# Kernel optimization log

Measured on AMD Instinct MI355X. Metric: run time of the kernel, lower is better.

The kernel has to match this reference:

```python
import jax, jax.numpy as jnp
import numpy as np

EPS = 1e-5

def conv2d(x, w, stride=1, padding=0, bias=None):
    out = jax.lax.conv_general_dilated(
        x, w, (stride, stride), [(padding, padding), (padding, padding)],
        dimension_numbers=('NCHW', 'OIHW', 'NCHW'))
    if bias is not None:
        out = out + bias[None, :, None, None]
    return out

def bn_relu(x, gamma, beta, mean, var):
    scale = gamma / jnp.sqrt(var + EPS)
    return jax.nn.relu(x * scale[None, :, None, None]
                       + (beta - mean * scale)[None, :, None, None])

def deform_conv(x, wp, bp, wc, ks, pad, stride):
    # Canonical DeformConv2d (v1, modulation=False) from pytorch-deform-conv-v2.
    b, c, H, W = x.shape
    N = ks * ks
    offset = conv2d(x, wp, stride=stride, padding=1, bias=bp)        # (b,2N,h,w)
    h, w = offset.shape[2], offset.shape[3]
    xp = jnp.pad(x, ((0, 0), (0, 0), (pad, pad), (pad, pad)))        # zero_padding
    Hp, Wp = H + 2 * pad, W + 2 * pad
    off = offset.transpose(0, 2, 3, 1)                               # (b,h,w,2N)
    rng = jnp.arange(-(ks - 1) // 2, (ks - 1) // 2 + 1, dtype=x.dtype)
    pnx, pny = jnp.meshgrid(rng, rng, indexing='ij')
    pnx, pny = pnx.reshape(-1), pny.reshape(-1)                      # (N,)
    p0x = jnp.arange(1, h * stride + 1, stride, dtype=x.dtype)       # torch starts at 1
    p0y = jnp.arange(1, w * stride + 1, stride, dtype=x.dtype)
    px = p0x[None, :, None, None] + pnx[None, None, None, :] + off[..., :N]  # (b,h,w,N)
    py = p0y[None, None, :, None] + pny[None, None, None, :] + off[..., N:]
    qx0 = jnp.floor(jax.lax.stop_gradient(px))
    qy0 = jnp.floor(jax.lax.stop_gradient(py))
    qx0c = jnp.clip(qx0, 0, Hp - 1).astype(jnp.int32)
    qx1c = jnp.clip(qx0 + 1, 0, Hp - 1).astype(jnp.int32)
    qy0c = jnp.clip(qy0, 0, Wp - 1).astype(jnp.int32)
    qy1c = jnp.clip(qy0 + 1, 0, Wp - 1).astype(jnp.int32)
    pxc = jnp.clip(px, 0, Hp - 1)
    pyc = jnp.clip(py, 0, Wp - 1)
    fx0 = qx0c.astype(x.dtype); fx1 = qx1c.astype(x.dtype)
    fy0 = qy0c.astype(x.dtype); fy1 = qy1c.astype(x.dtype)
    g_lt = (1 + (fx0 - pxc)) * (1 + (fy0 - pyc))
    g_rb = (1 - (fx1 - pxc)) * (1 - (fy1 - pyc))
    g_lb = (1 + (fx0 - pxc)) * (1 - (fy1 - pyc))
    g_rt = (1 - (fx1 - pxc)) * (1 + (fy0 - pyc))
    xf = xp.reshape(b, c, Hp * Wp)
    def gather(qx, qy):
        idx = (qx * Wp + qy).reshape(b, 1, h * w * N)
        return jnp.take_along_axis(xf, idx, axis=2).reshape(b, c, h, w, N)
    x_off = (g_lt[:, None] * gather(qx0c, qy0c)
             + g_rb[:, None] * gather(qx1c, qy1c)
             + g_lb[:, None] * gather(qx0c, qy1c)
             + g_rt[:, None] * gather(qx1c, qy0c))                   # (b,c,h,w,N)
    # stride=ks conv over the reshaped (h*ks, w*ks) map == einsum over sample slot n
    return jnp.einsum('bchwn,ocn->bohw', x_off, wc.reshape(wc.shape[0], c, N))

def setup_inputs() -> dict:
    key = jax.random.key(0)
    ks = iter(jax.random.split(key, 40))
    def nrm(shape, scale):
        return jax.random.normal(next(ks), shape, dtype=jnp.float32) * scale
    def he(shape):  # fan_in = prod of all but first dim
        return nrm(shape, float(np.sqrt(2.0 / np.prod(shape[1:]))))
    def bn(c):
        return (jnp.ones((c,), jnp.float32) + nrm((c,), 0.05),  # gamma
                nrm((c,), 0.05),                                 # beta
                nrm((c,), 0.1),                                  # running mean
                jax.random.uniform(next(ks), (c,), jnp.float32, 0.5, 1.5))  # var
    inp = {'x': jax.random.normal(next(ks), (256, 3, 32, 32), dtype=jnp.float32)}
    inp['w1'] = he((32, 3, 3, 3)); inp['b1'] = nrm((32,), 0.01)
    inp['g1'], inp['be1'], inp['m1'], inp['v1'] = bn(32)
    inp['wp2'] = nrm((18, 32, 3, 3), 0.01); inp['bp2'] = nrm((18,), 0.001)
    inp['wc2'] = he((64, 32, 3, 3))
    inp['g2'], inp['be2'], inp['m2'], inp['v2'] = bn(64)
    inp['wp3'] = nrm((18, 64, 3, 3), 0.01); inp['bp3'] = nrm((18,), 0.001)
    inp['wc3'] = he((128, 64, 3, 3))
    inp['g3'], inp['be3'], inp['m3'], inp['v3'] = bn(128)
    inp['wp4'] = nrm((18, 128, 3, 3), 0.01); inp['bp4'] = nrm((18,), 0.001)
    inp['wc4'] = he((128, 128, 3, 3))
    inp['g4'], inp['be4'], inp['m4'], inp['v4'] = bn(128)
    inp['wcls'] = nrm((100, 128), float(1.0 / np.sqrt(128)))
    inp['bcls'] = nrm((100,), 0.01)
    return inp

def reference(x, w1, b1, g1, be1, m1, v1,
              wp2, bp2, wc2, g2, be2, m2, v2,
              wp3, bp3, wc3, g3, be3, m3, v3,
              wp4, bp4, wc4, g4, be4, m4, v4,
              wcls, bcls):
    h = bn_relu(conv2d(x, w1, stride=1, padding=1, bias=b1), g1, be1, m1, v1)   # (b,32,32,32)
    h = bn_relu(deform_conv(h, wp2, bp2, wc2, 3, 1, 2), g2, be2, m2, v2)        # (b,64,16,16)
    h = bn_relu(deform_conv(h, wp3, bp3, wc3, 3, 1, 1), g3, be3, m3, v3)        # (b,128,16,16)
    h = bn_relu(deform_conv(h, wp4, bp4, wc4, 3, 1, 2), g4, be4, m4, v4)        # (b,128,8,8)
    h = jnp.mean(h, axis=(2, 3))                                                # avg_pool2d(8) -> (b,128)
    return h @ wcls.T + bcls[None, :]
```

## Files before the change

kernel.cpp:

```cpp
#include <hip/hip_runtime.h>
#include <math.h>

#define BN_EPS 1e-5f

typedef __attribute__((ext_vector_type(4))) float f4;
typedef __attribute__((ext_vector_type(4))) int i4v;
typedef __attribute__((ext_vector_type(8))) short short8;
typedef __attribute__((ext_vector_type(4))) float f32x4;

__device__ inline unsigned short f2bf(float f) {
    unsigned int u = __builtin_bit_cast(unsigned int, f);
    return (unsigned short)((u + 0x7FFFu + ((u >> 16) & 1u)) >> 16);
}
__device__ inline float blo(int u) { return __builtin_bit_cast(float, (int)(u << 16)); }
__device__ inline float bhi(int u) { return __builtin_bit_cast(float, (int)(u & 0xffff0000)); }
__device__ inline int pkbf_fast(float hi, float lo) {
    unsigned uh = __builtin_bit_cast(unsigned, hi) + 0x8000u;
    unsigned ul = __builtin_bit_cast(unsigned, lo) + 0x8000u;
    return (int)__builtin_amdgcn_perm(uh, ul, 0x07060302u);
}

struct CvtSeg { const float* src; unsigned short* dst; int oreal, c, kpad, end; };
struct CvtArgs { CvtSeg s[7]; };

__global__ __launch_bounds__(256)
void cvt_all(CvtArgs a)
{
    int idx = blockIdx.x * 256 + threadIdx.x;
    int base = 0;
    #pragma unroll
    for (int i = 0; i < 7; ++i) {
        if (idx < a.s[i].end) {
            int local = idx - base;
            int kpad = a.s[i].kpad, c = a.s[i].c;
            int o = local / kpad, k = local - o * kpad;
            unsigned short val = 0;
            if (o < a.s[i].oreal && k < 9 * c) {
                int n = k / c, cc = k - n * c;
                val = f2bf(a.s[i].src[(o * c + cc) * 9 + n]);
            }
            a.s[i].dst[local] = val;
            return;
        }
        base = a.s[i].end;
    }
}

__global__ __launch_bounds__(256)
void conv1_tile(const float* __restrict__ x, const unsigned short* __restrict__ wq,
                const float* __restrict__ bias, const float* __restrict__ g,
                const float* __restrict__ be, const float* __restrict__ m,
                const float* __restrict__ v, unsigned short* __restrict__ out)
{
    __shared__ __align__(16) float img[3072];
    __shared__ __align__(16) unsigned short wt[32 * 40];
    __shared__ float scb[32], shb[32];
    const int tid = threadIdx.x;
    const int b = blockIdx.x >> 2;
    const int qtr = blockIdx.x & 3;
    if (tid < 32) {
        float sc = g[tid] * rsqrtf(v[tid] + BN_EPS);
        scb[tid] = sc;
        shb[tid] = be[tid] - m[tid] * sc + bias[tid] * sc;
    }
    *(ushort4*)&wt[(tid >> 3) * 40 + (tid & 7) * 4] =
        *(const ushort4*)(wq + (tid >> 3) * 32 + (tid & 7) * 4);
    const float* xb = x + (size_t)b * 3072;
    #pragma unroll
    for (int r = 0; r < 3; ++r) {
        int idx = r * 256 + tid;
        *(f4*)&img[idx * 4] = *(const f4*)(xb + idx * 4);
    }
    __syncthreads();
    const int wid = tid >> 6, lane = tid & 63, quad = lane >> 4, m16 = lane & 15;
    short8 af0 = *(const short8*)&wt[m16 * 40 + quad * 8];
    short8 af1 = *(const short8*)&wt[(16 + m16) * 40 + quad * 8];
    #pragma unroll
    for (int it = 0; it < 4; ++it) {
        int pix = qtr * 256 + it * 64 + wid * 16 + m16;
        int i = pix >> 5, j = pix & 31;
        short8 bfrag;
        #pragma unroll
        for (int jj = 0; jj < 8; ++jj) {
            int k = quad * 8 + jj;
            float val = 0.f;
            if (k < 27) {
                int n = k / 3, c = k - n * 3;
                int u = i - 1 + n / 3, vv = j - 1 + n % 3;
                if (u >= 0 && u < 32 && vv >= 0 && vv < 32)
                    val = img[c * 1024 + u * 32 + vv];
            }
            bfrag[jj] = (short)f2bf(val);
        }
        f32x4 a0 = {0.f,0.f,0.f,0.f}, a1 = {0.f,0.f,0.f,0.f};
        a0 = __builtin_amdgcn_mfma_f32_16x16x32_bf16(af0, bfrag, a0, 0, 0, 0);
        a1 = __builtin_amdgcn_mfma_f32_16x16x32_bf16(af1, bfrag, a1, 0, 0, 0);
        unsigned short* op = out + ((size_t)b * 1024 + pix) * 32;
        ushort4 s0, s1;
        #pragma unroll
        for (int rr = 0; rr < 4; ++rr) {
            int o0 = quad * 4 + rr, o1 = 16 + quad * 4 + rr;
            ((unsigned short*)&s0)[rr] = f2bf(fmaxf(fmaf(a0[rr], scb[o0], shb[o0]), 0.f));
            ((unsigned short*)&s1)[rr] = f2bf(fmaxf(fmaf(a1[rr], scb[o1], shb[o1]), 0.f));
        }
        *(ushort4*)(op + quad * 4) = s0;
        *(ushort4*)(op + 16 + quad * 4) = s1;
    }
}

template<int C, int OREAL, int OPAD, int H, int W, int OH, int OW, int S,
         int MTILE, bool DEF, bool BN>
__global__ __launch_bounds__(256, 4)
void dconv(const unsigned short* __restrict__ xact, const float* __restrict__ offp,
           const unsigned short* __restrict__ wq,
           const float* __restrict__ q0, const float* __restrict__ q1,
           const float* __restrict__ q2, const float* __restrict__ q3,
           void* __restrict__ outv)
{
    constexpr int K = C * 9;
    constexpr int KCH = C / 32;
    constexpr int OSPLIT = (OPAD >= 64) ? 4 : 2;
    constexpr int G = 4 / OSPLIT;
    constexpr int OT = OPAD / (16 * OSPLIT);
    constexpr int PW = MTILE / G;
    constexpr int ST = PW / 16;
    constexpr int CP = C + 8;
    constexpr int GL = C / 8;
    constexpr int NGRP = 256 / GL;
    constexpr int NT_ITER = (MTILE + NGRP - 1) / NGRP;
    constexpr int OHW = OH * OW;
    constexpr int HWC = H * W * C;
    constexpr int Hp = H + 2, Wp = W + 2;
    static_assert(PW % 16 == 0 && OT >= 1 && MTILE % NGRP == 0, "tiling");

    __shared__ __align__(16) unsigned short xo[2][MTILE * CP];
    __shared__ __align__(16) i4v tab_i[DEF ? MTILE : 1][9];
    __shared__ __align__(16) f4  tab_w[DEF ? MTILE : 1][9];
    __shared__ int tab_o[DEF ? 1 : MTILE][9];
    __shared__ int tab_m[DEF ? 1 : MTILE][9];
    __shared__ int imgb[MTILE];
    __shared__ float scb[OPAD], shb[OPAD];

    const int tid = threadIdx.x;
    const int p0 = blockIdx.x * MTILE;

    if (tid < MTILE) imgb[tid] = ((p0 + tid) / OHW) * HWC;
    if (BN) {
        for (int o = tid; o < OREAL; o += 256) {
            float sc = q0[o] * rsqrtf(q3[o] + BN_EPS);
            scb[o] = sc;
            shb[o] = q1[o] - q2[o] * sc;
        }
    } else {
        for (int o = tid; o < OREAL; o += 256) scb[o] = q0[o];
    }

    for (int e = tid; e < MTILE * 9; e += 256) {
        int lp = e / 9, n = e % 9;
        int p = p0 + lp;
        int rem = p % OHW;
        int i = rem / OW, j = rem % OW;
        if constexpr (DEF) {
            float ox = offp[(size_t)p * 18 + n];
            float oy = offp[(size_t)p * 18 + 9 + n];
            float px = (float)(i * S + n / 3) + ox;
            float py = (float)(j * S + n % 3) + oy;
            int qx0 = (int)floorf(px), qy0 = (int)floorf(py);
            int x0 = min(max(qx0, 0), Hp - 1), x1 = min(max(qx0 + 1, 0), Hp - 1);
            int y0 = min(max(qy0, 0), Wp - 1), y1 = min(max(qy0 + 1, 0), Wp - 1);
            float pxc = fminf(fmaxf(px, 0.f), (float)(Hp - 1));
            float pyc = fminf(fmaxf(py, 0.f), (float)(Wp - 1));
            float gx0 = 1.f + ((float)x0 - pxc), gx1 = 1.f - ((float)x1 - pxc);
            float gy0 = 1.f + ((float)y0 - pyc), gy1 = 1.f - ((float)y1 - pyc);
            int u0 = x0 - 1, u1 = x1 - 1, v0 = y0 - 1, v1 = y1 - 1;
            bool k0 = (u0 >= 0 && u0 < H && v0 >= 0 && v0 < W);
            bool k1 = (u1 >= 0 && u1 < H && v1 >= 0 && v1 < W);
            bool k2 = (u0 >= 0 && u0 < H && v1 >= 0 && v1 < W);
            bool k3 = (u1 >= 0 && u1 < H && v0 >= 0 && v0 < W);
            i4v ti; f4 tw;
            ti[0] = k0 ? (u0 * W + v0) * C : 0;  tw[0] = k0 ? gx0 * gy0 : 0.f;
            ti[1] = k1 ? (u1 * W + v1) * C : 0;  tw[1] = k1 ? gx1 * gy1 : 0.f;
            ti[2] = k2 ? (u0 * W + v1) * C : 0;  tw[2] = k2 ? gx0 * gy1 : 0.f;
            ti[3] = k3 ? (u1 * W + v0) * C : 0;  tw[3] = k3 ? gx1 * gy0 : 0.f;
            tab_i[lp][n] = ti;
            tab_w[lp][n] = tw;
        } else {
            int u = i * S - 1 + n / 3, vv = j * S - 1 + n % 3;
            bool ok = (u >= 0 && u < H && vv >= 0 && vv < W);
            tab_o[lp][n] = ok ? (u * W + vv) * C : 0;
            tab_m[lp][n] = ok ? -1 : 0;
        }
    }

    const int gl = tid % GL;
    const int grp = tid / GL;
    const int wid = tid >> 6, lane = tid & 63, quad = lane >> 4, m16 = lane & 15;
    const int og = wid % OSPLIT, pg = wid / OSPLIT;
    const int obase = og * OT * 16;
    const int pixbase = pg * PW;

    auto do_gather = [&](int n, int buf) {
        #pragma unroll
        for (int it = 0; it < NT_ITER; ++it) {
            const int pix = it * NGRP + grp;
            const unsigned short* xb = xact + imgb[pix] + gl * 8;
            i4v R;
            if constexpr (DEF) {
                i4v ti = tab_i[pix][n];
                f4  tw = tab_w[pix][n];
                i4v A  = *(const i4v*)(xb + ti[0]);
                i4v Bv = *(const i4v*)(xb + ti[1]);
                i4v Cv = *(const i4v*)(xb + ti[2]);
                i4v Dv = *(const i4v*)(xb + ti[3]);
                #pragma unroll
                for (int e2 = 0; e2 < 4; ++e2) {
                    float lo = tw[0] * blo(A[e2]);
                    lo = fmaf(tw[1], blo(Bv[e2]), lo);
                    lo = fmaf(tw[2], blo(Cv[e2]), lo);
                    lo = fmaf(tw[3], blo(Dv[e2]), lo);
                    float hi = tw[0] * bhi(A[e2]);
                    hi = fmaf(tw[1], bhi(Bv[e2]), hi);
                    hi = fmaf(tw[2], bhi(Cv[e2]), hi);
                    hi = fmaf(tw[3], bhi(Dv[e2]), hi);
                    R[e2] = pkbf_fast(hi, lo);
                }
            } else {
                int mask = tab_m[pix][n];
                i4v A = *(const i4v*)(xb + tab_o[pix][n]);
                #pragma unroll
                for (int e2 = 0; e2 < 4; ++e2) R[e2] = A[e2] & mask;
            }
            *(i4v*)&xo[buf][pix * CP + gl * 8] = R;
        }
    };

    auto load_wf = [&](int n, short8 (*wf)[OT]) {
        #pragma unroll
        for (int ch = 0; ch < KCH; ++ch)
            #pragma unroll
            for (int t = 0; t < OT; ++t)
                wf[ch][t] = *(const short8*)(wq + (size_t)(obase + t * 16 + m16) * K
                                             + n * C + ch * 32 + quad * 8);
    };

    f32x4 acc[ST][OT];
    #pragma unroll
    for (int st = 0; st < ST; ++st)
        #pragma unroll
        for (int t = 0; t < OT; ++t) acc[st][t] = (f32x4){0.f, 0.f, 0.f, 0.f};

    short8 wfA[KCH][OT], wfB[KCH][OT];
    __syncthreads();
    do_gather(0, 0);
    load_wf(0, wfA);
    __syncthreads();

    for (int n = 0; n < 9; ++n) {
        const int cur = n & 1;
        if (n < 8) {
            do_gather(n + 1, cur ^ 1);
            load_wf(n + 1, wfB);
        }
        #pragma unroll
        for (int ch = 0; ch < KCH; ++ch)
            #pragma unroll
            for (int st = 0; st < ST; ++st) {
                short8 bf = *(const short8*)&xo[cur][(pixbase + st * 16 + m16) * CP
                                                    + ch * 32 + quad * 8];
                #pragma unroll
                for (int t = 0; t < OT; ++t)
                    acc[st][t] = __builtin_amdgcn_mfma_f32_16x16x32_bf16(
                        wfA[ch][t], bf, acc[st][t], 0, 0, 0);
            }
        if (n < 8) {
            #pragma unroll
            for (int ch = 0; ch < KCH; ++ch)
                #pragma unroll
                for (int t = 0; t < OT; ++t) wfA[ch][t] = wfB[ch][t];
        }
        __syncthreads();
    }

    if constexpr (BN) {
        unsigned short* outw = (unsigned short*)outv;
        #pragma unroll
        for (int st = 0; st < ST; ++st) {
            const int p = p0 + pixbase + st * 16 + m16;
            #pragma unroll
            for (int t = 0; t < OT; ++t) {
                int o = obase + t * 16 + quad * 4;
                ushort4 s;
                #pragma unroll
                for (int rr = 0; rr < 4; ++rr)
                    ((unsigned short*)&s)[rr] =
                        f2bf(fmaxf(fmaf(acc[st][t][rr], scb[o + rr], shb[o + rr]), 0.f));
                *(ushort4*)(outw + (size_t)p * OPAD + o) = s;
            }
        }
    } else {
        float* outf = (float*)outv;
        #pragma unroll
        for (int st = 0; st < ST; ++st) {
            const int p = p0 + pixbase + st * 16 + m16;
            #pragma unroll
            for (int t = 0; t < OT; ++t)
                #pragma unroll
                for (int rr = 0; rr < 4; ++rr) {
                    int o = obase + t * 16 + quad * 4 + rr;
                    if (o < OREAL)
                        outf[(size_t)p * 18 + o] = acc[st][t][rr] + scb[o];
                }
        }
    }
}

__global__ __launch_bounds__(128)
void pool_fc(const unsigned short* __restrict__ h4, const float* __restrict__ wcls,
             const float* __restrict__ bcls, float* __restrict__ out)
{
    __shared__ float pool[128];
    int b = blockIdx.x;
    int tid = threadIdx.x;
    const unsigned short* src = h4 + (size_t)b * 8192;
    float s = 0.f;
    #pragma unroll
    for (int t = 0; t < 64; ++t)
        s += __builtin_bit_cast(float, (unsigned)src[t * 128 + tid] << 16);
    pool[tid] = s * (1.f / 64.f);
    __syncthreads();
    if (tid < 100) {
        float acc = bcls[tid];
        const float* wr = wcls + tid * 128;
        #pragma unroll
        for (int c = 0; c < 128; ++c) acc = fmaf(pool[c], wr[c], acc);
        out[(size_t)b * 100 + tid] = acc;
    }
}

extern "C" void kernel_launch(void* const* d_in, const int* in_sizes, int n_in,
                              void* d_out, int out_size, void* d_ws, size_t ws_size,
                              hipStream_t stream)
{
    const float* x    = (const float*)d_in[0];
    const float* w1   = (const float*)d_in[1];
    const float* b1   = (const float*)d_in[2];
    const float* g1   = (const float*)d_in[3];
    const float* be1  = (const float*)d_in[4];
    const float* m1   = (const float*)d_in[5];
    const float* v1   = (const float*)d_in[6];
    const float* wp2  = (const float*)d_in[7];
    const float* bp2  = (const float*)d_in[8];
    const float* wc2  = (const float*)d_in[9];
    const float* g2   = (const float*)d_in[10];
    const float* be2  = (const float*)d_in[11];
    const float* m2   = (const float*)d_in[12];
    const float* v2   = (const float*)d_in[13];
    const float* wp3  = (const float*)d_in[14];
    const float* bp3  = (const float*)d_in[15];
    const float* wc3  = (const float*)d_in[16];
    const float* g3   = (const float*)d_in[17];
    const float* be3  = (const float*)d_in[18];
    const float* m3   = (const float*)d_in[19];
    const float* v3   = (const float*)d_in[20];
    const float* wp4  = (const float*)d_in[21];
    const float* bp4  = (const float*)d_in[22];
    const float* wc4  = (const float*)d_in[23];
    const float* g4   = (const float*)d_in[24];
    const float* be4  = (const float*)d_in[25];
    const float* m4   = (const float*)d_in[26];
    const float* v4   = (const float*)d_in[27];
    const float* wcls = (const float*)d_in[28];
    const float* bcls = (const float*)d_in[29];
    float* out = (float*)d_out;

    float* ws  = (float*)d_ws;
    float* off = ws;
    unsigned short* h1 = (unsigned short*)(off + 1179648);
    unsigned short* h2 = h1 + 8388608;
    unsigned short* h3 = h2 + 4194304;
    unsigned short* h4 = h3 + 8388608;
    unsigned short* wc2b = h4 + 2097152;
    unsigned short* wc3b = wc2b + 18432;
    unsigned short* wc4b = wc3b + 73728;
    unsigned short* wp2b = wc4b + 147456;
    unsigned short* wp3b = wp2b + 9216;
    unsigned short* wp4b = wp3b + 18432;
    unsigned short* wq1  = wp4b + 36864;
    (void)ws_size; (void)in_sizes; (void)n_in; (void)out_size;

    CvtArgs ca;
    ca.s[0] = { wc2, wc2b, 64, 32, 288, 18432 };
    ca.s[1] = { wc3, wc3b, 128, 64, 576, 92160 };
    ca.s[2] = { wc4, wc4b, 128, 128, 1152, 239616 };
    ca.s[3] = { wp2, wp2b, 18, 32, 288, 248832 };
    ca.s[4] = { wp3, wp3b, 18, 64, 576, 267264 };
    ca.s[5] = { wp4, wp4b, 18, 128, 1152, 304128 };
    ca.s[6] = { w1, wq1, 32, 3, 32, 305152 };
    cvt_all<<<1192, 256, 0, stream>>>(ca);

    conv1_tile<<<1024, 256, 0, stream>>>(x, wq1, b1, g1, be1, m1, v1, h1);

    dconv<32, 18, 32, 32, 32, 16, 16, 2, 64, false, false><<<1024, 256, 0, stream>>>(
        h1, nullptr, wp2b, bp2, nullptr, nullptr, nullptr, off);
    dconv<32, 64, 64, 32, 32, 16, 16, 2, 64, true, true><<<1024, 256, 0, stream>>>(
        h1, off, wc2b, g2, be2, m2, v2, h2);

    dconv<64, 18, 32, 16, 16, 16, 16, 1, 64, false, false><<<1024, 256, 0, stream>>>(
        h2, nullptr, wp3b, bp3, nullptr, nullptr, nullptr, off);
    dconv<64, 128, 128, 16, 16, 16, 16, 1, 64, true, true><<<1024, 256, 0, stream>>>(
        h2, off, wc3b, g3, be3, m3, v3, h3);

    dconv<128, 18, 32, 16, 16, 8, 8, 2, 32, false, false><<<512, 256, 0, stream>>>(
        h3, nullptr, wp4b, bp4, nullptr, nullptr, nullptr, off);
    dconv<128, 128, 128, 16, 16, 8, 8, 2, 32, true, true><<<512, 256, 0, stream>>>(
        h3, off, wc4b, g4, be4, m4, v4, h4);

    pool_fc<<<256, 128, 0, stream>>>(h4, wcls, bcls, out);
}
```

Before: 241.8 us.

## Split gather into issue/commit phases to overlap global loads with MFMA

The deformable/im2col gather is split into an issue phase that loads the four bilinear corner vectors into registers, and a commit phase that blends and writes them to LDS after the current tap's MFMAs. This is meant to hide global-load latency behind the matrix compute instead of stalling on it before the MFMAs start. Because the loaded values now stay live across the MFMA loop, register pressure rises, so the launch bounds drop to 3 blocks per SM for deformable layers. NT_ITER is also simplified to an exact division, which the existing static_assert already guarantees.

Measured after the change: 239.8 us. Within noise of the previous version (-0.8%).

```diff
diff --git a/kernel.cpp b/kernel.cpp
--- a/kernel.cpp
+++ b/kernel.cpp
@@ -110,7 +110,7 @@
 
 template<int C, int OREAL, int OPAD, int H, int W, int OH, int OW, int S,
          int MTILE, bool DEF, bool BN>
-__global__ __launch_bounds__(256, 4)
+__global__ __launch_bounds__(256, DEF ? 3 : 4)
 void dconv(const unsigned short* __restrict__ xact, const float* __restrict__ offp,
            const unsigned short* __restrict__ wq,
            const float* __restrict__ q0, const float* __restrict__ q1,
@@ -127,7 +127,7 @@
     constexpr int CP = C + 8;
     constexpr int GL = C / 8;
     constexpr int NGRP = 256 / GL;
-    constexpr int NT_ITER = (MTILE + NGRP - 1) / NGRP;
+    constexpr int NT_ITER = MTILE / NGRP;
     constexpr int OHW = OH * OW;
     constexpr int HWC = H * W * C;
     constexpr int Hp = H + 2, Wp = W + 2;
@@ -199,36 +199,47 @@
     const int obase = og * OT * 16;
     const int pixbase = pg * PW;
 
-    auto do_gather = [&](int n, int buf) {
+    i4v T[NT_ITER][DEF ? 4 : 1];
+
+    auto gather_issue = [&](int n) {
         #pragma unroll
         for (int it = 0; it < NT_ITER; ++it) {
             const int pix = it * NGRP + grp;
             const unsigned short* xb = xact + imgb[pix] + gl * 8;
+            if constexpr (DEF) {
+                i4v ti = tab_i[pix][n];
+                T[it][0] = *(const i4v*)(xb + ti[0]);
+                T[it][1] = *(const i4v*)(xb + ti[1]);
+                T[it][2] = *(const i4v*)(xb + ti[2]);
+                T[it][3] = *(const i4v*)(xb + ti[3]);
+            } else {
+                T[it][0] = *(const i4v*)(xb + tab_o[pix][n]);
+            }
+        }
+    };
+    auto gather_commit = [&](int n, int buf) {
+        #pragma unroll
+        for (int it = 0; it < NT_ITER; ++it) {
+            const int pix = it * NGRP + grp;
             i4v R;
             if constexpr (DEF) {
-                i4v ti = tab_i[pix][n];
-                f4  tw = tab_w[pix][n];
-                i4v A  = *(const i4v*)(xb + ti[0]);
-                i4v Bv = *(const i4v*)(xb + ti[1]);
-                i4v Cv = *(const i4v*)(xb + ti[2]);
-                i4v Dv = *(const i4v*)(xb + ti[3]);
+                f4 tw = tab_w[pix][n];
                 #pragma unroll
                 for (int e2 = 0; e2 < 4; ++e2) {
-                    float lo = tw[0] * blo(A[e2]);
-                    lo = fmaf(tw[1], blo(Bv[e2]), lo);
-                    lo = fmaf(tw[2], blo(Cv[e2]), lo);
-                    lo = fmaf(tw[3], blo(Dv[e2]), lo);
-                    float hi = tw[0] * bhi(A[e2]);
-                    hi = fmaf(tw[1], bhi(Bv[e2]), hi);
-                    hi = fmaf(tw[2], bhi(Cv[e2]), hi);
-                    hi = fmaf(tw[3], bhi(Dv[e2]), hi);
+                    float lo = tw[0] * blo(T[it][0][e2]);
+                    lo = fmaf(tw[1], blo(T[it][1][e2]), lo);
+                    lo = fmaf(tw[2], blo(T[it][2][e2]), lo);
+                    lo = fmaf(tw[3], blo(T[it][3][e2]), lo);
+                    float hi = tw[0] * bhi(T[it][0][e2]);
+                    hi = fmaf(tw[1], bhi(T[it][1][e2]), hi);
+                    hi = fmaf(tw[2], bhi(T[it][2][e2]), hi);
+                    hi = fmaf(tw[3], bhi(T[it][3][e2]), hi);
                     R[e2] = pkbf_fast(hi, lo);
                 }
             } else {
                 int mask = tab_m[pix][n];
-                i4v A = *(const i4v*)(xb + tab_o[pix][n]);
-                #pragma unroll
-                for (int e2 = 0; e2 < 4; ++e2) R[e2] = A[e2] & mask;
+                #pragma unroll
+                for (int e2 = 0; e2 < 4; ++e2) R[e2] = T[it][0][e2] & mask;
             }
             *(i4v*)&xo[buf][pix * CP + gl * 8] = R;
         }
@@ -251,14 +262,15 @@
 
     short8 wfA[KCH][OT], wfB[KCH][OT];
     __syncthreads();
-    do_gather(0, 0);
+    gather_issue(0);
     load_wf(0, wfA);
+    gather_commit(0, 0);
     __syncthreads();
 
     for (int n = 0; n < 9; ++n) {
         const int cur = n & 1;
         if (n < 8) {
-            do_gather(n + 1, cur ^ 1);
+            gather_issue(n + 1);
             load_wf(n + 1, wfB);
         }
         #pragma unroll
@@ -273,6 +285,7 @@
                         wfA[ch][t], bf, acc[st][t], 0, 0, 0);
             }
         if (n < 8) {
+            gather_commit(n + 1, cur ^ 1);
             #pragma unroll
             for (int ch = 0; ch < KCH; ++ch)
                 #pragma unroll
```
